# Performance work log

Hardware: AMD Instinct MI355X
Metric: run time of the kernel (lower is better)

The kernel has to match this reference:

```python
import jax, jax.numpy as jnp
import numpy as np

MUL = 32            # multiplicity of each irrep
N_NODES = 16384
N_EDGES = 262144
AVG_NEIGH = 16.0
N_SPECIES = 4
RADIAL_DIM = 8
INV_SQRT3 = 0.5773502691896258  # normalized CG coeff for 1o x 1o -> 0e (dot)


def setup_inputs() -> dict:
    key = jax.random.key(0)
    ks = jax.random.split(key, 14)
    f32 = jnp.float32
    return {
        "node_features": jax.random.normal(ks[0], (N_NODES, 4 * MUL), dtype=f32),
        "edge_sh": jax.random.normal(ks[1], (N_EDGES, 4), dtype=f32),
        "radial_embedding": jax.random.uniform(ks[2], (N_EDGES, RADIAL_DIM), dtype=f32),
        "W_up_s": jax.random.normal(ks[3], (MUL, MUL), dtype=f32),
        "W_up_v": jax.random.normal(ks[4], (MUL, MUL), dtype=f32),
        "W_r1": jax.random.normal(ks[5], (RADIAL_DIM, RADIAL_DIM), dtype=f32),
        "W_r2": jax.random.normal(ks[6], (RADIAL_DIM, 4 * MUL), dtype=f32),
        "W_dn_s": jax.random.normal(ks[7], (2 * MUL, 2 * MUL), dtype=f32),
        "W_dn_v": jax.random.normal(ks[8], (2 * MUL, MUL), dtype=f32),
        "W_sk_s": jax.random.normal(ks[9], (N_SPECIES, MUL, 2 * MUL), dtype=f32),
        "W_sk_v": jax.random.normal(ks[10], (N_SPECIES, MUL, MUL), dtype=f32),
        "senders": jax.random.randint(ks[11], (N_EDGES,), 0, N_NODES),
        "receivers": jax.random.randint(ks[12], (N_EDGES,), 0, N_NODES),
        "node_species": jax.random.randint(ks[13], (N_NODES,), 0, N_SPECIES),
    }


def reference(node_features, edge_sh, radial_embedding, W_up_s, W_up_v,
              W_r1, W_r2, W_dn_s, W_dn_v, W_sk_s, W_sk_v,
              senders, receivers, node_species):
    n = node_features.shape[0]
    # irreps layout: 32x0e (first MUL cols) + 32x1o (next 3*MUL cols)
    s = node_features[:, :MUL]                      # [N, mul]     0e
    v = node_features[:, MUL:].reshape(n, MUL, 3)   # [N, mul, 3]  1o

    # linear_up: per-irrep channel mixing, 1/sqrt(fan_in) normalization
    s1 = (s @ W_up_s) * (MUL ** -0.5)
    v1 = jnp.einsum('nmi,mk->nki', v, W_up_v) * (MUL ** -0.5)

    # gather sender features per edge
    ss = s1[senders]              # [E, mul]
    vs = v1[senders]              # [E, mul, 3]
    yv = edge_sh[:, 1:4]          # 1o part of edge spherical harmonics (0e part dropped in TP)

    # Clebsch-Gordan tensor product, filtered to output irreps {0e, 1o}:
    #   0e x 1o -> 1o ;  1o x 1o -> 0e (dot, coeff 1/sqrt(3)); cross(1e) & 2e dropped
    m_v_tp = ss[:, :, None] * yv[:, None, :]                 # [E, mul, 3]
    m_s_tp = jnp.einsum('emi,ei->em', vs, yv) * INV_SQRT3    # [E, mul]

    # radial MLP -> one scalar weight per irrep instance of the message
    h = jax.nn.silu((radial_embedding @ W_r1) * (RADIAL_DIM ** -0.5))
    w = (h @ W_r2) * (RADIAL_DIM ** -0.5)                    # [E, 4*mul]
    w_ss, w_vs, w_vt, w_st = jnp.split(w, 4, axis=1)

    # message = concat(self-features, tensor-product paths), radially weighted
    m_s = jnp.concatenate([ss * w_ss, m_s_tp * w_st], axis=1)                          # [E, 2*mul]
    m_v = jnp.concatenate([vs * w_vs[:, :, None], m_v_tp * w_vt[:, :, None]], axis=1)  # [E, 2*mul, 3]

    # scatter-add into receiver nodes, divide by sqrt(avg_num_neighbours)
    inv = AVG_NEIGH ** -0.5
    S = jax.ops.segment_sum(m_s, receivers, num_segments=n) * inv                     # [N, 2*mul]
    V = jax.ops.segment_sum(m_v.reshape(m_v.shape[0], -1), receivers,
                            num_segments=n).reshape(n, 2 * MUL, 3) * inv              # [N, 2*mul, 3]

    # linear_down to gate irreps: MUL 0e features + MUL gate scalars, MUL 1o vectors
    g_s = (S @ W_dn_s) * ((2 * MUL) ** -0.5)                                          # [N, 2*mul]
    g_v = jnp.einsum('nmi,mk->nki', V, W_dn_v) * ((2 * MUL) ** -0.5)                  # [N, mul, 3]

    # species-indexed skip connection from the original node features
    sk_s = jnp.einsum('nm,nmk->nk', s, W_sk_s[node_species]) * (MUL ** -0.5)
    sk_v = jnp.einsum('nmi,nmk->nki', v, W_sk_v[node_species]) * (MUL ** -0.5)
    g_s = 0.5 * (g_s + sk_s)
    g_v = 0.5 * (g_v + sk_v)

    # gate nonlinearity: silu on even scalars, silu(gates) multiplies each 1o vector
    feat_s = jax.nn.silu(g_s[:, :MUL])
    gates = jax.nn.silu(g_s[:, MUL:])
    out_v = g_v * gates[:, :, None]
    return jnp.concatenate([feat_s, out_v.reshape(n, 3 * MUL)], axis=1)  # [N, 4*mul]
```

## Files before the change

kernel.cpp:

```cpp
#include <hip/hip_runtime.h>
#include <hip/hip_bf16.h>
#include <hip/hip_fp16.h>

#define N_NODES 16384
#define N_EDGES 262144
#define MUL 32
#define REC_CAP (N_EDGES + 3 * N_NODES + 16)

#if defined(__has_builtin)
#if __has_builtin(__builtin_amdgcn_fdot2)
#define HAS_FDOT2 1
#endif
#endif

typedef _Float16 h2_t __attribute__((ext_vector_type(2)));

__device__ __forceinline__ float silu_f(float x) {
    return x / (1.0f + __expf(-x));
}
__device__ __forceinline__ __half2 i2h2(int v) { return __builtin_bit_cast(__half2, v); }
__device__ __forceinline__ int h22i(__half2 v) { return __builtin_bit_cast(int, v); }
__device__ __forceinline__ h2_t mkh2(float a, float b) {
    h2_t r; r[0] = (_Float16)a; r[1] = (_Float16)b; return r;
}
__device__ __forceinline__ float dot2(int hbits, h2_t w, float acc) {
#ifdef HAS_FDOT2
    return __builtin_amdgcn_fdot2(__builtin_bit_cast(h2_t, hbits), w, acc, false);
#else
    float2 h = __half22float2(i2h2(hbits));
    return acc + h.x * (float)w[0] + h.y * (float)w[1];
#endif
}

__global__ void k_up(const float* __restrict__ nf,
                     const float* __restrict__ Wus,
                     const float* __restrict__ Wuv,
                     __half* __restrict__ up_h,
                     const int* __restrict__ recv,
                     int* __restrict__ counts,
                     int* __restrict__ rank) {
    __shared__ float sh[2][128];
    int node0 = blockIdx.x * 2;
    int t = threadIdx.x;
    if (t < 32) {
        int e = blockIdx.x * 32 + t;
        rank[e] = atomicAdd(&counts[recv[e]], 1);
    }
    sh[t >> 7][t & 127] = nf[(size_t)node0 * 128 + t];
    __syncthreads();
    int local = t >> 7;
    int c = t & 127;
    int m = c >> 2, comp = c & 3;
    const float* row = sh[local];
    float acc = 0.f;
    if (comp == 0) {
        #pragma unroll
        for (int k = 0; k < 32; ++k) acc += row[k] * Wus[k * 32 + m];
    } else {
        int i = comp - 1;
        #pragma unroll
        for (int k = 0; k < 32; ++k) acc += row[32 + k * 3 + i] * Wuv[k * 32 + m];
    }
    up_h[(size_t)(node0 + local) * 128 + c] = __float2half(acc * 0.17677669529663687f);
}

__global__ void k_scan(const int* __restrict__ counts,
                       int* __restrict__ starts) {
    __shared__ int wtot[16];
    __shared__ int woff[16];
    int t = threadIdx.x;
    int lane = t & 63, wid = t >> 6;
    const int4* cp = (const int4*)(counts + t * 16);
    int4 c0 = cp[0], c1 = cp[1], c2 = cp[2], c3 = cp[3];
    int cs[16] = {c0.x,c0.y,c0.z,c0.w,c1.x,c1.y,c1.z,c1.w,
                  c2.x,c2.y,c2.z,c2.w,c3.x,c3.y,c3.z,c3.w};
    int mysum = 0;
    #pragma unroll
    for (int i = 0; i < 16; ++i) {
        cs[i] = (cs[i] + 3) & ~3;
        mysum += cs[i];
    }
    int incl = mysum;
    #pragma unroll
    for (int off = 1; off < 64; off <<= 1) {
        int y = __shfl_up(incl, off, 64);
        if (lane >= off) incl += y;
    }
    if (lane == 63) wtot[wid] = incl;
    __syncthreads();
    if (t == 0) {
        int run = 0;
        #pragma unroll
        for (int w = 0; w < 16; ++w) { woff[w] = run; run += wtot[w]; }
    }
    __syncthreads();
    int run = woff[wid] + (incl - mysum);
    #pragma unroll
    for (int i = 0; i < 16; ++i) {
        starts[t * 16 + i] = run;
        run += cs[i];
    }
    if (t == 1023) starts[N_NODES] = run;
}

__global__ void k_edges(const float* __restrict__ rad,
                        const float* __restrict__ Wr1,
                        const int* __restrict__ recv,
                        const int* __restrict__ senders,
                        const float* __restrict__ esh,
                        const int* __restrict__ starts,
                        const int* __restrict__ counts,
                        const int* __restrict__ rank,
                        int4* __restrict__ records,
                        const float* __restrict__ Wdns,
                        const float* __restrict__ Wdnv,
                        const float* __restrict__ Wsks,
                        const float* __restrict__ Wskv,
                        float4* __restrict__ pk_dn,
                        float4* __restrict__ pk_sk) {
    int e = blockIdx.x * blockDim.x + threadIdx.x;
    const int4 z = make_int4(0, 0, 0, 0);

    if (e < 2048) {
        int mm = e >> 5, m0 = e & 31;
        pk_dn[e] = make_float4(Wdns[mm * 64 + m0], Wdns[mm * 64 + 32 + m0],
                               Wdnv[mm * 32 + m0], 0.f);
    } else if (e < 6144) {
        int j = e - 2048;
        int sp = j >> 10, mm = (j >> 5) & 31, m0 = j & 31;
        pk_sk[j] = make_float4(Wsks[sp * 2048 + mm * 64 + m0],
                               Wsks[sp * 2048 + mm * 64 + 32 + m0],
                               Wskv[sp * 1024 + mm * 32 + m0], 0.f);
    }

    if (e < N_NODES) {
        int st = starts[e] + counts[e];
        int en = starts[e + 1];
        for (int p = st; p < en; ++p) {
            records[2 * (size_t)p] = z;
            records[2 * (size_t)p + 1] = z;
        }
    }
    if (e < 16) {
        int total = starts[N_NODES];
        records[2 * (size_t)(total + e)] = z;
        records[2 * (size_t)(total + e) + 1] = z;
    }

    const float4* rp = (const float4*)(rad + (size_t)e * 8);
    float4 a = rp[0], b = rp[1];
    float r[8] = {a.x, a.y, a.z, a.w, b.x, b.y, b.z, b.w};
    float h[8];
    #pragma unroll
    for (int j = 0; j < 8; ++j) {
        float acc = 0.f;
        #pragma unroll
        for (int k = 0; k < 8; ++k) acc += r[k] * Wr1[k * 8 + j];
        h[j] = silu_f(acc * 0.35355339059327373f);
    }
    float4 ey = *(const float4*)(esh + (size_t)e * 4);
    int snd = senders[e];
    int rc = recv[e];
    int pos = starts[rc] + rank[e];
    int4 meta;
    meta.x = snd;
    meta.y = h22i(__floats2half2_rn(ey.y, ey.z));
    meta.z = h22i(__floats2half2_rn(ey.w, 0.f));
    meta.w = 0;
    int4 hp;
    hp.x = h22i(__floats2half2_rn(h[0], h[1]));
    hp.y = h22i(__floats2half2_rn(h[2], h[3]));
    hp.z = h22i(__floats2half2_rn(h[4], h[5]));
    hp.w = h22i(__floats2half2_rn(h[6], h[7]));
    records[2 * (size_t)pos] = meta;
    records[2 * (size_t)pos + 1] = hp;
}

struct Acc {
    float S0, S1, Vv0, Vv1, Vv2, Vt0, Vt1, Vt2;
};
__device__ __forceinline__ void edge_accum(int4 meta, int4 hp, int2 q,
                                           const h2_t* __restrict__ w2a,
                                           const h2_t* __restrict__ w2b,
                                           const h2_t* __restrict__ w2c,
                                           const h2_t* __restrict__ w2d,
                                           Acc& A) {
    float wss = dot2(hp.x, w2a[0], dot2(hp.y, w2a[1], dot2(hp.z, w2a[2], dot2(hp.w, w2a[3], 0.f))));
    float wvs = dot2(hp.x, w2b[0], dot2(hp.y, w2b[1], dot2(hp.z, w2b[2], dot2(hp.w, w2b[3], 0.f))));
    float wvt = dot2(hp.x, w2c[0], dot2(hp.y, w2c[1], dot2(hp.z, w2c[2], dot2(hp.w, w2c[3], 0.f))));
    float wst = dot2(hp.x, w2d[0], dot2(hp.y, w2d[1], dot2(hp.z, w2d[2], dot2(hp.w, w2d[3], 0.f))));

    float2 y01 = __half22float2(i2h2(meta.y));
    float2 y2p = __half22float2(i2h2(meta.z));
    float y0 = y01.x, y1 = y01.y, y2 = y2p.x;
    float2 sv0 = __half22float2(i2h2(q.x));
    float2 v12 = __half22float2(i2h2(q.y));
    float ss = sv0.x, v0 = sv0.y, v1v = v12.x, v2 = v12.y;
    float dot = v0 * y0 + v1v * y1 + v2 * y2;
    A.S0 += ss * wss;
    A.S1 += dot * wst;
    A.Vv0 += v0 * wvs; A.Vv1 += v1v * wvs; A.Vv2 += v2 * wvs;
    float tv = ss * wvt;
    A.Vt0 += tv * y0; A.Vt1 += tv * y1; A.Vt2 += tv * y2;
}

__launch_bounds__(256, 6)
__global__ void k_gather(const __half* __restrict__ up_h,
                         const float* __restrict__ nf,
                         const int4* __restrict__ records,
                         const float* __restrict__ Wr2,
                         const int* __restrict__ starts,
                         const float4* __restrict__ pk_dn,
                         const float4* __restrict__ pk_sk,
                         const int* __restrict__ species,
                         float* __restrict__ out) {
    __shared__ float4 agg4[4][64];
    __shared__ float4 sk4[4][32];

    int tid = threadIdx.x;
    int w = tid >> 6;
    int lane = tid & 63;
    int sub = lane >> 5;
    int m = lane & 31;
    int node = blockIdx.x * 4 + w;

    int s0 = starts[node], s1 = starts[node + 1];

    int ta = s0 + sub;
    const int4* rp;
    rp = records + 2 * (size_t)ta;        int4 c0 = rp[0], c1 = rp[1];
    rp = records + 2 * (size_t)(ta + 2);  int4 d0 = rp[0], d1 = rp[1];

    if (lane < 32) {
        const float* src = nf + (size_t)node * 128;
        float s = src[lane];
        float a0 = src[32 + 3 * lane + 0];
        float a1 = src[32 + 3 * lane + 1];
        float a2 = src[32 + 3 * lane + 2];
        sk4[w][lane] = make_float4(s, a0, a1, a2);
    }

    int2 qa = *(const int2*)(up_h + (size_t)c0.x * 128 + m * 4);
    int2 qb = *(const int2*)(up_h + (size_t)d0.x * 128 + m * 4);

    rp = records + 2 * (size_t)(ta + 4);  int4 n0 = rp[0], n1 = rp[1];
    rp = records + 2 * (size_t)(ta + 6);  int4 e0 = rp[0], e1 = rp[1];

    const float s8 = 0.35355339059327373f;
    const float s8s3 = 0.35355339059327373f * 0.5773502691896258f;
    h2_t w2a[4], w2b[4], w2c[4], w2d[4];
    #pragma unroll
    for (int j4 = 0; j4 < 4; ++j4) {
        int j = 2 * j4;
        w2a[j4] = mkh2(Wr2[j * 128 + m] * s8,        Wr2[(j + 1) * 128 + m] * s8);
        w2b[j4] = mkh2(Wr2[j * 128 + 32 + m] * s8,   Wr2[(j + 1) * 128 + 32 + m] * s8);
        w2c[j4] = mkh2(Wr2[j * 128 + 64 + m] * s8,   Wr2[(j + 1) * 128 + 64 + m] * s8);
        w2d[j4] = mkh2(Wr2[j * 128 + 96 + m] * s8s3, Wr2[(j + 1) * 128 + 96 + m] * s8s3);
    }

    Acc A = {0.f,0.f,0.f,0.f,0.f,0.f,0.f,0.f};
    Acc B = {0.f,0.f,0.f,0.f,0.f,0.f,0.f,0.f};

    #pragma unroll 1
    for (int t0 = s0; t0 < s1; t0 += 4) {
        int2 qna = *(const int2*)(up_h + (size_t)n0.x * 128 + m * 4);
        int2 qnb = *(const int2*)(up_h + (size_t)e0.x * 128 + m * 4);

        int t2 = t0 + 8 + sub;
        rp = records + 2 * (size_t)t2;        int4 p0 = rp[0], p1 = rp[1];
        rp = records + 2 * (size_t)(t2 + 2);  int4 r0 = rp[0], r1 = rp[1];

        edge_accum(c0, c1, qa, w2a, w2b, w2c, w2d, A);
        edge_accum(d0, d1, qb, w2a, w2b, w2c, w2d, B);

        c0 = n0; c1 = n1; d0 = e0; d1 = e1;
        qa = qna; qb = qnb;
        n0 = p0; n1 = p1; e0 = r0; e1 = r1;
    }

    float accS0 = A.S0 + B.S0, accS1 = A.S1 + B.S1;
    float accVv0 = A.Vv0 + B.Vv0, accVv1 = A.Vv1 + B.Vv1, accVv2 = A.Vv2 + B.Vv2;
    float accVt0 = A.Vt0 + B.Vt0, accVt1 = A.Vt1 + B.Vt1, accVt2 = A.Vt2 + B.Vt2;

    accS0 += __shfl_xor(accS0, 32, 64);
    accS1 += __shfl_xor(accS1, 32, 64);
    accVv0 += __shfl_xor(accVv0, 32, 64);
    accVv1 += __shfl_xor(accVv1, 32, 64);
    accVv2 += __shfl_xor(accVv2, 32, 64);
    accVt0 += __shfl_xor(accVt0, 32, 64);
    accVt1 += __shfl_xor(accVt1, 32, 64);
    accVt2 += __shfl_xor(accVt2, 32, 64);

    const float inv_neigh = 0.25f;
    if (sub == 0) {
        agg4[w][m]      = make_float4(accS0 * inv_neigh, accVv0 * inv_neigh,
                                      accVv1 * inv_neigh, accVv2 * inv_neigh);
        agg4[w][32 + m] = make_float4(accS1 * inv_neigh, accVt0 * inv_neigh,
                                      accVt1 * inv_neigh, accVt2 * inv_neigh);
    }

    int sp = species[node];

    float gsa = 0.f, gsb = 0.f, gv0 = 0.f, gv1 = 0.f, gv2 = 0.f;
    {
        const float4* agp = agg4[w];
        int mm0 = sub * 32;
        #pragma unroll 4
        for (int k = 0; k < 32; ++k) {
            int mm = mm0 + k;
            float4 sv = agp[mm];
            float4 wq = pk_dn[mm * 32 + m];
            gsa += sv.x * wq.x;
            gsb += sv.x * wq.y;
            gv0 += sv.y * wq.z;
            gv1 += sv.z * wq.z;
            gv2 += sv.w * wq.z;
        }
    }
    float ska = 0.f, skb = 0.f, skv0 = 0.f, skv1 = 0.f, skv2 = 0.f;
    {
        const float4* pks = pk_sk + (size_t)sp * 1024;
        int mm0 = sub * 16;
        #pragma unroll 4
        for (int k = 0; k < 16; ++k) {
            int mm = mm0 + k;
            float4 sv = sk4[w][mm];
            float4 wq = pks[mm * 32 + m];
            ska += sv.x * wq.x;
            skb += sv.x * wq.y;
            skv0 += sv.y * wq.z;
            skv1 += sv.z * wq.z;
            skv2 += sv.w * wq.z;
        }
    }
    gsa += __shfl_xor(gsa, 32, 64);
    gsb += __shfl_xor(gsb, 32, 64);
    gv0 += __shfl_xor(gv0, 32, 64);
    gv1 += __shfl_xor(gv1, 32, 64);
    gv2 += __shfl_xor(gv2, 32, 64);
    ska += __shfl_xor(ska, 32, 64);
    skb += __shfl_xor(skb, 32, 64);
    skv0 += __shfl_xor(skv0, 32, 64);
    skv1 += __shfl_xor(skv1, 32, 64);
    skv2 += __shfl_xor(skv2, 32, 64);

    if (sub == 0) {
        const float inv8 = 0.125f;
        const float isq32 = 0.17677669529663687f;
        float a  = 0.5f * (gsa * inv8 + ska * isq32);
        float b  = 0.5f * (gsb * inv8 + skb * isq32);
        float o0 = 0.5f * (gv0 * inv8 + skv0 * isq32);
        float o1 = 0.5f * (gv1 * inv8 + skv1 * isq32);
        float o2 = 0.5f * (gv2 * inv8 + skv2 * isq32);

        float feat = silu_f(a);
        float gate = silu_f(b);
        float* o = out + (size_t)node * 128;
        o[m] = feat;
        o[32 + 3 * m + 0] = o0 * gate;
        o[32 + 3 * m + 1] = o1 * gate;
        o[32 + 3 * m + 2] = o2 * gate;
    }
}

extern "C" void kernel_launch(void* const* d_in, const int* in_sizes, int n_in,
                              void* d_out, int out_size, void* d_ws, size_t ws_size,
                              hipStream_t stream) {
    const float* nf   = (const float*)d_in[0];
    const float* esh  = (const float*)d_in[1];
    const float* rad  = (const float*)d_in[2];
    const float* Wus  = (const float*)d_in[3];
    const float* Wuv  = (const float*)d_in[4];
    const float* Wr1  = (const float*)d_in[5];
    const float* Wr2  = (const float*)d_in[6];
    const float* Wdns = (const float*)d_in[7];
    const float* Wdnv = (const float*)d_in[8];
    const float* Wsks = (const float*)d_in[9];
    const float* Wskv = (const float*)d_in[10];
    const int* senders   = (const int*)d_in[11];
    const int* receivers = (const int*)d_in[12];
    const int* species   = (const int*)d_in[13];
    float* out = (float*)d_out;

    char* ws = (char*)d_ws;
    __half* up_h   = (__half*)(ws);
    int4* records  = (int4*)(ws + (4u << 20));
    int* counts    = (int*)(ws + (14u << 20));
    int* starts    = (int*)(ws + (14u << 20) + 65536);
    int* rank      = (int*)(ws + (15u << 20));
    float4* pk_dn  = (float4*)(ws + (16u << 20));
    float4* pk_sk  = (float4*)(ws + (16u << 20) + 32768);

    hipMemsetAsync(counts, 0, 65536, stream);
    k_up<<<N_NODES / 2, 256, 0, stream>>>(nf, Wus, Wuv, up_h, receivers, counts, rank);
    k_scan<<<1, 1024, 0, stream>>>(counts, starts);
    k_edges<<<N_EDGES / 256, 256, 0, stream>>>(rad, Wr1, receivers, senders, esh,
                                               starts, counts, rank, records,
                                               Wdns, Wdnv, Wsks, Wskv, pk_dn, pk_sk);
    k_gather<<<N_NODES / 4, 256, 0, stream>>>(up_h, nf, records, Wr2, starts,
                                              pk_dn, pk_sk, species, out);
}
```

Before: 174.5 us.

## Split each node's edge gather across two wavefronts and combine via shared memory

The gather kernel now assigns two wavefronts per node, each handling alternating groups of four edges, doubling the grid size. Partial aggregates are written to shared memory, combined after a block barrier, and only two of the four wavefronts run the down-projection, skip connection and gating epilogue. The record padding grows to cover the deeper prefetch distance. This targets latency of the per-node edge loop, at the cost of a __syncthreads and half the waves sitting idle during the epilogue.

```diff
diff --git a/kernel.cpp b/kernel.cpp
--- a/kernel.cpp
+++ b/kernel.cpp
@@ -5,7 +5,7 @@
 #define N_NODES 16384
 #define N_EDGES 262144
 #define MUL 32
-#define REC_CAP (N_EDGES + 3 * N_NODES + 16)
+#define REC_CAP (N_EDGES + 3 * N_NODES + 24)
 
 #if defined(__has_builtin)
 #if __has_builtin(__builtin_amdgcn_fdot2)
@@ -141,7 +141,7 @@
             records[2 * (size_t)p + 1] = z;
         }
     }
-    if (e < 16) {
+    if (e < 24) {
         int total = starts[N_NODES];
         records[2 * (size_t)(total + e)] = z;
         records[2 * (size_t)(total + e) + 1] = z;
@@ -214,37 +214,39 @@
                          const float4* __restrict__ pk_sk,
                          const int* __restrict__ species,
                          float* __restrict__ out) {
-    __shared__ float4 agg4[4][64];
-    __shared__ float4 sk4[4][32];
+    __shared__ float4 aggp[2][2][64];
+    __shared__ float4 sk4[2][32];
 
     int tid = threadIdx.x;
     int w = tid >> 6;
     int lane = tid & 63;
     int sub = lane >> 5;
     int m = lane & 31;
-    int node = blockIdx.x * 4 + w;
+    int nslot = w >> 1;
+    int pair = w & 1;
+    int node = blockIdx.x * 2 + nslot;
 
     int s0 = starts[node], s1 = starts[node + 1];
 
-    int ta = s0 + sub;
+    int ta = s0 + 4 * pair + sub;
     const int4* rp;
     rp = records + 2 * (size_t)ta;        int4 c0 = rp[0], c1 = rp[1];
     rp = records + 2 * (size_t)(ta + 2);  int4 d0 = rp[0], d1 = rp[1];
 
-    if (lane < 32) {
+    if (pair == 0 && lane < 32) {
         const float* src = nf + (size_t)node * 128;
         float s = src[lane];
         float a0 = src[32 + 3 * lane + 0];
         float a1 = src[32 + 3 * lane + 1];
         float a2 = src[32 + 3 * lane + 2];
-        sk4[w][lane] = make_float4(s, a0, a1, a2);
+        sk4[nslot][lane] = make_float4(s, a0, a1, a2);
     }
 
     int2 qa = *(const int2*)(up_h + (size_t)c0.x * 128 + m * 4);
     int2 qb = *(const int2*)(up_h + (size_t)d0.x * 128 + m * 4);
 
-    rp = records + 2 * (size_t)(ta + 4);  int4 n0 = rp[0], n1 = rp[1];
-    rp = records + 2 * (size_t)(ta + 6);  int4 e0 = rp[0], e1 = rp[1];
+    rp = records + 2 * (size_t)(ta + 8);   int4 n0 = rp[0], n1 = rp[1];
+    rp = records + 2 * (size_t)(ta + 10);  int4 e0 = rp[0], e1 = rp[1];
 
     const float s8 = 0.35355339059327373f;
     const float s8s3 = 0.35355339059327373f * 0.5773502691896258f;
@@ -262,13 +264,12 @@
     Acc B = {0.f,0.f,0.f,0.f,0.f,0.f,0.f,0.f};
 
     #pragma unroll 1
-    for (int t0 = s0; t0 < s1; t0 += 4) {
+    for (int t0 = s0 + 4 * pair; t0 < s1; t0 += 8) {
         int2 qna = *(const int2*)(up_h + (size_t)n0.x * 128 + m * 4);
         int2 qnb = *(const int2*)(up_h + (size_t)e0.x * 128 + m * 4);
 
-        int t2 = t0 + 8 + sub;
-        rp = records + 2 * (size_t)t2;        int4 p0 = rp[0], p1 = rp[1];
-        rp = records + 2 * (size_t)(t2 + 2);  int4 r0 = rp[0], r1 = rp[1];
+        rp = records + 2 * (size_t)(ta + 16);  int4 p0 = rp[0], p1 = rp[1];
+        rp = records + 2 * (size_t)(ta + 18);  int4 r0 = rp[0], r1 = rp[1];
 
         edge_accum(c0, c1, qa, w2a, w2b, w2c, w2d, A);
         edge_accum(d0, d1, qb, w2a, w2b, w2c, w2d, B);
@@ -276,6 +277,7 @@
         c0 = n0; c1 = n1; d0 = e0; d1 = e1;
         qa = qna; qb = qnb;
         n0 = p0; n1 = p1; e0 = r0; e1 = r1;
+        ta += 8;
     }
 
     float accS0 = A.S0 + B.S0, accS1 = A.S1 + B.S1;
@@ -293,73 +295,81 @@
 
     const float inv_neigh = 0.25f;
     if (sub == 0) {
-        agg4[w][m]      = make_float4(accS0 * inv_neigh, accVv0 * inv_neigh,
-                                      accVv1 * inv_neigh, accVv2 * inv_neigh);
-        agg4[w][32 + m] = make_float4(accS1 * inv_neigh, accVt0 * inv_neigh,
-                                      accVt1 * inv_neigh, accVt2 * inv_neigh);
-    }
-
-    int sp = species[node];
-
-    float gsa = 0.f, gsb = 0.f, gv0 = 0.f, gv1 = 0.f, gv2 = 0.f;
-    {
-        const float4* agp = agg4[w];
-        int mm0 = sub * 32;
-        #pragma unroll 4
-        for (int k = 0; k < 32; ++k) {
-            int mm = mm0 + k;
-            float4 sv = agp[mm];
-            float4 wq = pk_dn[mm * 32 + m];
-            gsa += sv.x * wq.x;
-            gsb += sv.x * wq.y;
-            gv0 += sv.y * wq.z;
-            gv1 += sv.z * wq.z;
-            gv2 += sv.w * wq.z;
+        aggp[nslot][pair][m]      = make_float4(accS0 * inv_neigh, accVv0 * inv_neigh,
+                                                accVv1 * inv_neigh, accVv2 * inv_neigh);
+        aggp[nslot][pair][32 + m] = make_float4(accS1 * inv_neigh, accVt0 * inv_neigh,
+                                                accVt1 * inv_neigh, accVt2 * inv_neigh);
+    }
+    __syncthreads();
+
+    if (w < 2) {
+        int enode = blockIdx.x * 2 + w;
+        int sp = species[enode];
+
+        float gsa = 0.f, gsb = 0.f, gv0 = 0.f, gv1 = 0.f, gv2 = 0.f;
+        {
+            const float4* p0 = aggp[w][0];
+            const float4* p1 = aggp[w][1];
+            int mm0 = sub * 32;
+            #pragma unroll 4
+            for (int k = 0; k < 32; ++k) {
+                int mm = mm0 + k;
+                float4 a0 = p0[mm];
+                float4 a1 = p1[mm];
+                float4 sv = make_float4(a0.x + a1.x, a0.y + a1.y,
+                                        a0.z + a1.z, a0.w + a1.w);
+                float4 wq = pk_dn[mm * 32 + m];
+                gsa += sv.x * wq.x;
+                gsb += sv.x * wq.y;
+                gv0 += sv.y * wq.z;
+                gv1 += sv.z * wq.z;
+                gv2 += sv.w * wq.z;
+            }
         }
-    }
-    float ska = 0.f, skb = 0.f, skv0 = 0.f, skv1 = 0.f, skv2 = 0.f;
-    {
-        const float4* pks = pk_sk + (size_t)sp * 1024;
-        int mm0 = sub * 16;
-        #pragma unroll 4
-        for (int k = 0; k < 16; ++k) {
-            int mm = mm0 + k;
-            float4 sv = sk4[w][mm];
-            float4 wq = pks[mm * 32 + m];
-            ska += sv.x * wq.x;
-            skb += sv.x * wq.y;
-            skv0 += sv.y * wq.z;
-            skv1 += sv.z * wq.z;
-            skv2 += sv.w * wq.z;
+        float ska = 0.f, skb = 0.f, skv0 = 0.f, skv1 = 0.f, skv2 = 0.f;
+        {
+            const float4* pks = pk_sk + (size_t)sp * 1024;
+            int mm0 = sub * 16;
+            #pragma unroll 4
+            for (int k = 0; k < 16; ++k) {
+                int mm = mm0 + k;
+                float4 sv = sk4[w][mm];
+                float4 wq = pks[mm * 32 + m];
+                ska += sv.x * wq.x;
+                skb += sv.x * wq.y;
+                skv0 += sv.y * wq.z;
+                skv1 += sv.z * wq.z;
+                skv2 += sv.w * wq.z;
+            }
         }
-    }
-    gsa += __shfl_xor(gsa, 32, 64);
-    gsb += __shfl_xor(gsb, 32, 64);
-    gv0 += __shfl_xor(gv0, 32, 64);
-    gv1 += __shfl_xor(gv1, 32, 64);
-    gv2 += __shfl_xor(gv2, 32, 64);
-    ska += __shfl_xor(ska, 32, 64);
-    skb += __shfl_xor(skb, 32, 64);
-    skv0 += __shfl_xor(skv0, 32, 64);
-    skv1 += __shfl_xor(skv1, 32, 64);
-    skv2 += __shfl_xor(skv2, 32, 64);
-
-    if (sub == 0) {
-        const float inv8 = 0.125f;
-        const float isq32 = 0.17677669529663687f;
-        float a  = 0.5f * (gsa * inv8 + ska * isq32);
-        float b  = 0.5f * (gsb * inv8 + skb * isq32);
-        float o0 = 0.5f * (gv0 * inv8 + skv0 * isq32);
-        float o1 = 0.5f * (gv1 * inv8 + skv1 * isq32);
-        float o2 = 0.5f * (gv2 * inv8 + skv2 * isq32);
-
-        float feat = silu_f(a);
-        float gate = silu_f(b);
-        float* o = out + (size_t)node * 128;
-        o[m] = feat;
-        o[32 + 3 * m + 0] = o0 * gate;
-        o[32 + 3 * m + 1] = o1 * gate;
-        o[32 + 3 * m + 2] = o2 * gate;
+        gsa += __shfl_xor(gsa, 32, 64);
+        gsb += __shfl_xor(gsb, 32, 64);
+        gv0 += __shfl_xor(gv0, 32, 64);
+        gv1 += __shfl_xor(gv1, 32, 64);
+        gv2 += __shfl_xor(gv2, 32, 64);
+        ska += __shfl_xor(ska, 32, 64);
+        skb += __shfl_xor(skb, 32, 64);
+        skv0 += __shfl_xor(skv0, 32, 64);
+        skv1 += __shfl_xor(skv1, 32, 64);
+        skv2 += __shfl_xor(skv2, 32, 64);
+
+        if (sub == 0) {
+            const float inv8 = 0.125f;
+            const float isq32 = 0.17677669529663687f;
+            float a  = 0.5f * (gsa * inv8 + ska * isq32);
+            float b  = 0.5f * (gsb * inv8 + skb * isq32);
+            float o0 = 0.5f * (gv0 * inv8 + skv0 * isq32);
+            float o1 = 0.5f * (gv1 * inv8 + skv1 * isq32);
+            float o2 = 0.5f * (gv2 * inv8 + skv2 * isq32);
+
+            float feat = silu_f(a);
+            float gate = silu_f(b);
+            float* o = out + (size_t)enode * 128;
+            o[m] = feat;
+            o[32 + 3 * m + 0] = o0 * gate;
+            o[32 + 3 * m + 1] = o1 * gate;
+            o[32 + 3 * m + 2] = o2 * gate;
+        }
     }
 }
 
@@ -397,6 +407,6 @@
     k_edges<<<N_EDGES / 256, 256, 0, stream>>>(rad, Wr1, receivers, senders, esh,
                                                starts, counts, rank, records,
                                                Wdns, Wdnv, Wsks, Wskv, pk_dn, pk_sk);
-    k_gather<<<N_NODES / 4, 256, 0, stream>>>(up_h, nf, records, Wr2, starts,
+    k_gather<<<N_NODES / 2, 256, 0, stream>>>(up_h, nf, records, Wr2, starts,
                                               pk_dn, pk_sk, species, out);
 }
```

After: 179.8 us. +3.0%, slower.
